# Optimization experiments

Measured on AMD Instinct MI355X. Metric: run time of the kernel, lower is better.

## Reference

```python
import jax, jax.numpy as jnp
import numpy as np

B, D, K = 4, 64, 32
T, H, W = 8, 32, 32


def setup_inputs() -> dict:
    key = jax.random.key(0)
    k1, k2, k3, k4, k5 = jax.random.split(key, 5)
    std1 = 1.0 / float(np.sqrt(K * D))
    X = jax.random.normal(k1, (B, D, T, H, W), dtype=jnp.float32)
    codewords = jax.random.uniform(k2, (K, D), dtype=jnp.float32, minval=-std1, maxval=std1)
    scale = jax.random.uniform(k3, (K, D), dtype=jnp.float32, minval=-1.0, maxval=0.0)
    fc_w = jax.random.normal(k4, (D, D), dtype=jnp.float32) * (1.0 / np.sqrt(D))
    fc_b = jax.random.normal(k5, (D,), dtype=jnp.float32) * 0.01
    return {"X": X, "codewords": codewords, "scale": scale, "fc_w": fc_w, "fc_b": fc_b}


def reference(X, codewords, scale, fc_w, fc_b):
    b, d, t, h, w = X.shape
    n = t * h * w
    # (B, N, D) voxel features
    I = X.reshape(b, d, n).transpose(0, 2, 1)
    # residuals to each codeword: (B, N, K, D)
    resid = I[:, :, None, :] - codewords[None, None, :, :]
    # scaled squared-distance softmax over K (per feature channel d)
    A = jax.nn.softmax(scale[None, None, :, :] * jnp.square(resid), axis=2)
    AR = A * resid  # (B, N, K, D)
    # aggregate over voxels -> (B, K, D), then mean over codewords -> (B, D)
    E_glob = AR.sum(axis=1).mean(axis=1)
    gamma = jax.nn.sigmoid(E_glob @ fc_w.T + fc_b)  # (B, D)
    # aggregate over codewords -> (B, N, D) -> (B, D, T, H, W)
    E = AR.sum(axis=2).transpose(0, 2, 1).reshape(b, d, t, h, w)
    return jax.nn.relu(E + E * gamma[:, :, None, None, None])
```

## Files before the change

kernel.cpp:

```cpp
#include <hip/hip_runtime.h>
#include <hip/hip_bf16.h>

#define BB 4
#define DD 64
#define KK 32
#define NN 8192
#define LOG2E 1.4426950408889634f

__global__ __launch_bounds__(256) void enc_kernel(
    const float* __restrict__ X,
    const float* __restrict__ cw,
    const float* __restrict__ sc,
    float* __restrict__ E,
    float* __restrict__ eglob)
{
    const int bd   = blockIdx.x >> 3;
    const int nblk = blockIdx.x & 7;
    const int d    = bd & (DD - 1);
    const int n    = nblk * 1024 + (threadIdx.x << 2);
    const int idx  = bd * NN + n;

    const float4 x = *(const float4*)(X + idx);

    float num0 = 0.f, num1 = 0.f, num2 = 0.f, num3 = 0.f;
    float den0 = 0.f, den1 = 0.f, den2 = 0.f, den3 = 0.f;

#pragma unroll
    for (int k = 0; k < KK; ++k) {
        const float c = cw[k * DD + d];
        const float s = sc[k * DD + d] * LOG2E;
        const float r0 = x.x - c;
        const float r1 = x.y - c;
        const float r2 = x.z - c;
        const float r3 = x.w - c;
        const float e0 = exp2f(s * r0 * r0);
        const float e1 = exp2f(s * r1 * r1);
        const float e2 = exp2f(s * r2 * r2);
        const float e3 = exp2f(s * r3 * r3);
        den0 += e0; num0 = fmaf(e0, r0, num0);
        den1 += e1; num1 = fmaf(e1, r1, num1);
        den2 += e2; num2 = fmaf(e2, r2, num2);
        den3 += e3; num3 = fmaf(e3, r3, num3);
    }

    float4 out;
    out.x = num0 / den0;
    out.y = num1 / den1;
    out.z = num2 / den2;
    out.w = num3 / den3;
    *(float4*)(E + idx) = out;

    float t = out.x + out.y + out.z + out.w;
#pragma unroll
    for (int off = 32; off > 0; off >>= 1)
        t += __shfl_down(t, off);

    __shared__ float smem[4];
    const int lane = threadIdx.x & 63;
    const int wv   = threadIdx.x >> 6;
    if (lane == 0) smem[wv] = t;
    __syncthreads();
    if (threadIdx.x == 0) {
        const float bs = smem[0] + smem[1] + smem[2] + smem[3];
        atomicAdd(&eglob[bd], bs);
    }
}

__global__ __launch_bounds__(256) void gamma_kernel(
    const float* __restrict__ eglob,
    const float* __restrict__ fcw,
    const float* __restrict__ fcb,
    float* __restrict__ gamma)
{
    const int bd = threadIdx.x;
    const int b  = bd >> 6;
    const int d  = bd & (DD - 1);
    float acc = fcb[d];
    const float invK = 1.0f / (float)KK;
#pragma unroll
    for (int j = 0; j < DD; ++j)
        acc = fmaf(eglob[b * DD + j] * invK, fcw[d * DD + j], acc);
    gamma[bd] = 1.0f / (1.0f + __expf(-acc));
}

__global__ __launch_bounds__(256) void out_kernel(
    float* __restrict__ E,
    const float* __restrict__ gamma)
{
    const int bd  = blockIdx.x >> 3;
    const int idx = bd * NN + (blockIdx.x & 7) * 1024 + (threadIdx.x << 2);
    const float g = 1.0f + gamma[bd];
    float4 e = *(float4*)(E + idx);
    e.x = fmaxf(e.x * g, 0.f);
    e.y = fmaxf(e.y * g, 0.f);
    e.z = fmaxf(e.z * g, 0.f);
    e.w = fmaxf(e.w * g, 0.f);
    *(float4*)(E + idx) = e;
}

extern "C" void kernel_launch(void* const* d_in, const int* in_sizes, int n_in,
                              void* d_out, int out_size, void* d_ws, size_t ws_size,
                              hipStream_t stream) {
    const float* X   = (const float*)d_in[0];
    const float* cw  = (const float*)d_in[1];
    const float* sc  = (const float*)d_in[2];
    const float* fcw = (const float*)d_in[3];
    const float* fcb = (const float*)d_in[4];
    float* out = (float*)d_out;

    float* eglob = (float*)d_ws;
    float* gamma = eglob + BB * DD;

    hipMemsetAsync(eglob, 0, BB * DD * sizeof(float), stream);

    const int grid = BB * DD * (NN / 1024);
    enc_kernel<<<grid, 256, 0, stream>>>(X, cw, sc, out, eglob);
    gamma_kernel<<<1, 256, 0, stream>>>(eglob, fcw, fcb, gamma);
    out_kernel<<<grid, 256, 0, stream>>>(out, gamma);
}
```

Measured before the change: 96.57 us.

## Fuse gamma computation into output kernel and replace atomics with per-block partials

The encoding kernel now writes one partial sum per block instead of atomically adding into a global accumulator, which removes the memset and the atomics. The separate single-block gamma kernel is folded into the output kernel. Each block reduces the partials for its batch into shared memory and recomputes the 64-term dot product and sigmoid for its channel. This cuts two launches and a serialized tiny kernel, at the cost of redundant per-block gate computation.

```diff
diff --git a/kernel.cpp b/kernel.cpp
--- a/kernel.cpp
+++ b/kernel.cpp
@@ -12,13 +12,11 @@
     const float* __restrict__ cw,
     const float* __restrict__ sc,
     float* __restrict__ E,
-    float* __restrict__ eglob)
+    float* __restrict__ partial)
 {
     const int bd   = blockIdx.x >> 3;
-    const int nblk = blockIdx.x & 7;
     const int d    = bd & (DD - 1);
-    const int n    = nblk * 1024 + (threadIdx.x << 2);
-    const int idx  = bd * NN + n;
+    const int idx  = bd * NN + (blockIdx.x & 7) * 1024 + (threadIdx.x << 2);
 
     const float4 x = *(const float4*)(X + idx);
 
@@ -56,41 +54,39 @@
         t += __shfl_down(t, off);
 
     __shared__ float smem[4];
-    const int lane = threadIdx.x & 63;
-    const int wv   = threadIdx.x >> 6;
-    if (lane == 0) smem[wv] = t;
+    if ((threadIdx.x & 63) == 0) smem[threadIdx.x >> 6] = t;
     __syncthreads();
-    if (threadIdx.x == 0) {
-        const float bs = smem[0] + smem[1] + smem[2] + smem[3];
-        atomicAdd(&eglob[bd], bs);
-    }
+    if (threadIdx.x == 0)
+        partial[blockIdx.x] = smem[0] + smem[1] + smem[2] + smem[3];
 }
 
-__global__ __launch_bounds__(256) void gamma_kernel(
-    const float* __restrict__ eglob,
+__global__ __launch_bounds__(256) void gate_kernel(
+    float* __restrict__ E,
+    const float* __restrict__ partial,
     const float* __restrict__ fcw,
-    const float* __restrict__ fcb,
-    float* __restrict__ gamma)
+    const float* __restrict__ fcb)
 {
-    const int bd = threadIdx.x;
-    const int b  = bd >> 6;
-    const int d  = bd & (DD - 1);
-    float acc = fcb[d];
-    const float invK = 1.0f / (float)KK;
+    const int bd  = blockIdx.x >> 3;
+    const int b   = bd >> 6;
+    const int d   = bd & (DD - 1);
+    const int idx = bd * NN + (blockIdx.x & 7) * 1024 + (threadIdx.x << 2);
+
+    __shared__ float eg[DD];
+    if (threadIdx.x < DD) {
+        const float4* p = (const float4*)(partial + b * 512 + threadIdx.x * 8);
+        const float4 a = p[0], c4 = p[1];
+        eg[threadIdx.x] = (a.x + a.y + a.z + a.w) + (c4.x + c4.y + c4.z + c4.w);
+    }
+    float4 e = *(float4*)(E + idx);
+    __syncthreads();
+
+    float acc = 0.f;
 #pragma unroll
     for (int j = 0; j < DD; ++j)
-        acc = fmaf(eglob[b * DD + j] * invK, fcw[d * DD + j], acc);
-    gamma[bd] = 1.0f / (1.0f + __expf(-acc));
-}
+        acc = fmaf(eg[j], fcw[d * DD + j], acc);
+    const float z = acc * (1.0f / (float)KK) + fcb[d];
+    const float g = 1.0f + 1.0f / (1.0f + exp2f(-z * LOG2E));
 
-__global__ __launch_bounds__(256) void out_kernel(
-    float* __restrict__ E,
-    const float* __restrict__ gamma)
-{
-    const int bd  = blockIdx.x >> 3;
-    const int idx = bd * NN + (blockIdx.x & 7) * 1024 + (threadIdx.x << 2);
-    const float g = 1.0f + gamma[bd];
-    float4 e = *(float4*)(E + idx);
     e.x = fmaxf(e.x * g, 0.f);
     e.y = fmaxf(e.y * g, 0.f);
     e.z = fmaxf(e.z * g, 0.f);
@@ -108,13 +104,9 @@
     const float* fcb = (const float*)d_in[4];
     float* out = (float*)d_out;
 
-    float* eglob = (float*)d_ws;
-    float* gamma = eglob + BB * DD;
-
-    hipMemsetAsync(eglob, 0, BB * DD * sizeof(float), stream);
+    float* partial = (float*)d_ws;
 
     const int grid = BB * DD * (NN / 1024);
-    enc_kernel<<<grid, 256, 0, stream>>>(X, cw, sc, out, eglob);
-    gamma_kernel<<<1, 256, 0, stream>>>(eglob, fcw, fcb, gamma);
-    out_kernel<<<grid, 256, 0, stream>>>(out, gamma);
+    enc_kernel<<<grid, 256, 0, stream>>>(X, cw, sc, out, partial);
+    gate_kernel<<<grid, 256, 0, stream>>>(out, partial, fcw, fcb);
 }
```

Measured after the change: 90.48 us. 6.3% less time.
